# Kernel optimization log

Measured on AMD Instinct MI355X. Metric: run time of the kernel, lower is better.

## Reference

```python
import jax, jax.numpy as jnp
import numpy as np

N, E, IN, H = 10000, 50000, 32, 64


def setup_inputs() -> dict:
    key = jax.random.key(0)
    ks = jax.random.split(key, 12)
    s = lambda k, sh, sc=0.1: jax.random.normal(k, sh, dtype=jnp.float32) * sc
    return {
        "x": jax.random.normal(ks[0], (N, IN), dtype=jnp.float32),
        "edge_index": jax.random.randint(ks[1], (2, E), 0, N),
        "edge_attr": jax.random.uniform(ks[2], (E, 4), dtype=jnp.float32),
        "lin0_w": s(ks[3], (IN, H)),
        "lin0_b": jnp.zeros((H,), jnp.float32),
        "nn_w": s(ks[4], (4, H * H), 0.05),
        "nn_b": jnp.zeros((H * H,), jnp.float32),
        "root_w": s(ks[5], (H, H)),
        "conv_b": jnp.zeros((H,), jnp.float32),
        "gru_w_ih": s(ks[6], (3 * H, H)),
        "gru_w_hh": s(ks[7], (3 * H, H)),
        "gru_b_ih": jnp.zeros((3 * H,), jnp.float32),
        "gru_b_hh": jnp.zeros((3 * H,), jnp.float32),
    }


def reference(x, edge_index, edge_attr, lin0_w, lin0_b, nn_w, nn_b, root_w,
              conv_b, gru_w_ih, gru_w_hh, gru_b_ih, gru_b_hh):
    src, dst = edge_index[0], edge_index[1]
    # part == 'R': initial embedding
    out = jax.nn.relu(x @ lin0_w + lin0_b)  # [N, H]
    # Edge-conditioned weights are identical across the 3 iterations -> compute once.
    theta = (edge_attr @ nn_w + nn_b).reshape(E, H, H)  # per-edge [in, out]
    h = out  # GRU hidden init = out (h = out.unsqueeze(0))
    for _ in range(3):
        # NNConv: gather -> per-edge matmul -> scatter-add, plus root weight & bias
        msg = jnp.einsum('ei,eio->eo', out[src], theta)            # [E, H]
        agg = jax.ops.segment_sum(msg, dst, num_segments=N)        # [N, H]
        m = jax.nn.relu(agg + out @ root_w + conv_b)               # [N, H]
        # torch.nn.GRU single step (seq_len=1)
        gi = m @ gru_w_ih.T + gru_b_ih                             # [N, 3H]
        gh = h @ gru_w_hh.T + gru_b_hh                             # [N, 3H]
        i_r, i_z, i_n = jnp.split(gi, 3, axis=-1)
        h_r, h_z, h_n = jnp.split(gh, 3, axis=-1)
        r = jax.nn.sigmoid(i_r + h_r)
        z = jax.nn.sigmoid(i_z + h_z)
        n = jnp.tanh(i_n + r * h_n)
        h = (1.0 - z) * n + z * h
        out = h
    return out
```

## Files before the change

kernel.cpp:

```cpp
#include <hip/hip_runtime.h>


#define CAP 24
#define PACKB 96

using bf16x8 = __attribute__((ext_vector_type(8))) short;
using f32x4  = __attribute__((ext_vector_type(4))) float;

__device__ __forceinline__ float sigmoidf_(float x) { return 1.0f / (1.0f + __expf(-x)); }
__device__ __forceinline__ float tanhf_(float x) { return 2.0f / (1.0f + __expf(-2.0f * x)) - 1.0f; }
__device__ __forceinline__ unsigned short bf16r(float f) {
    unsigned u = __float_as_uint(f);
    return (unsigned short)((u + 0x7fffu + ((u >> 16) & 1u)) >> 16);
}
__device__ __forceinline__ unsigned bf16pk(float lo, float hi) {
    return (unsigned)bf16r(lo) | ((unsigned)bf16r(hi) << 16);
}

__global__ __launch_bounds__(256) void combo_k(const float* __restrict__ x,
                                               const float* __restrict__ w0,
                                               const float* __restrict__ b0,
                                               const float* __restrict__ nn_w,
                                               const float* __restrict__ nn_b,
                                               const float* __restrict__ root_w,
                                               const float* __restrict__ w_ih,
                                               const float* __restrict__ w_hh,
                                               unsigned* __restrict__ Wpk,
                                               float* __restrict__ h,
                                               int* __restrict__ dcnt, int N) {
    const int bid = blockIdx.x, tid = threadIdx.x;
    if (bid < PACKB) {
        int idx = bid * 256 + tid;
        int l = (idx >> 2) & 63, p = idx & 3;
        int kq = ((l >> 4) << 3) + 2 * p;
        float v0, v1;
        if (idx < 12288) {
            int f = idx >> 8;
            int ct = f / 12, s = f % 12;
            int k = 32 * s + kq;
            int col = 16 * ct + (l & 15);
            int c = k >> 6, j = k & 63;
            const float* base = (c < 4) ? nn_w + c * 4096 : (c == 4) ? nn_b : root_w;
            v0 = base[j * 64 + col];
            v1 = base[(j + 1) * 64 + col];
        } else {
            int idx2 = idx - 12288;
            int ts = idx2 >> 8;
            int g = ts >> 4, ct = (ts >> 2) & 3, s = ts & 3;
            int k = 32 * s + kq;
            int col = 16 * ct + (l & 15);
            const float* src = (k < 64) ? w_ih : w_hh;
            int kk = k & 63;
            v0 = src[(g * 64 + col) * 64 + kk];
            v1 = src[(g * 64 + col) * 64 + kk + 1];
        }
        Wpk[idx] = bf16pk(v0, v1);
    } else {
        int gid = (bid - PACKB) * 256 + tid;
        int gsz = (gridDim.x - PACKB) * 256;
        for (int i = gid; i < N; i += gsz) dcnt[i] = 0;
        for (int idx = gid; idx < N * 64; idx += gsz) {
            int n = idx >> 6, l = idx & 63;
            float acc = b0[l];
#pragma unroll
            for (int j = 0; j < 32; ++j) acc = fmaf(x[n * 32 + j], w0[j * 64 + l], acc);
            h[idx] = fmaxf(acc, 0.0f);
        }
    }
}

__global__ __launch_bounds__(256) void fillell_k(const int* __restrict__ ei,
                                                 const float4* __restrict__ ea,
                                                 int* __restrict__ dcnt,
                                                 int* __restrict__ esrc,
                                                 float4* __restrict__ eattr, int E) {
    int e = blockIdx.x * 256 + threadIdx.x;
    if (e >= E) return;
    int d = ei[E + e];
    int pos = atomicAdd(dcnt + d, 1);
    if (pos < CAP) {
        esrc[d * CAP + pos] = ei[e];
        eattr[d * CAP + pos] = ea[e];
    }
}

__global__ __launch_bounds__(256, 2) void iter_k(const float* __restrict__ h_old,
                                                 float* __restrict__ h_new,
                                                 const int* __restrict__ dcnt,
                                                 const int* __restrict__ esrc,
                                                 const float4* __restrict__ eattr,
                                                 const unsigned* __restrict__ Wpk,
                                                 const float* __restrict__ conv_b,
                                                 const float* __restrict__ b_ih,
                                                 const float* __restrict__ b_hh,
                                                 float* __restrict__ out_final, int N) {
    __shared__ unsigned short A1[16 * 384];
    __shared__ unsigned short AC[16 * 128];
    const int tid = threadIdx.x;
    const int n0 = blockIdx.x * 16;
    const int lane = tid & 63, wv = tid >> 6;

    bf16x8 wb[12], wc[12];
#pragma unroll
    for (int s = 0; s < 12; ++s)
        wb[s] = *(const bf16x8*)(Wpk + (wv * 12 + s) * 256 + lane * 4);
#pragma unroll
    for (int t = 0; t < 12; ++t) {
        int g = t >> 2, s = t & 3;
        wc[t] = *(const bf16x8*)(Wpk + 12288 + ((g * 4 + wv) * 4 + s) * 256 + lane * 4);
    }

    {
        int r = tid >> 4, q = tid & 15;
        int n = n0 + r;
        float4 hv = (n < N) ? *(const float4*)(h_old + (size_t)n * 64 + q * 4)
                            : make_float4(0.f, 0.f, 0.f, 0.f);
        uint2 pp = make_uint2(bf16pk(hv.x, hv.y), bf16pk(hv.z, hv.w));
        int sg1 = (40 + (q >> 1)) ^ (r & 7);
        *(uint2*)(A1 + r * 384 + sg1 * 8 + (q & 1) * 4) = pp;
        int sg2 = (8 + (q >> 1)) ^ (r & 7);
        *(uint2*)(AC + r * 128 + sg2 * 8 + (q & 1) * 4) = pp;
    }

#pragma unroll
    for (int i = 0; i < 4; ++i) {
        int r = wv * 4 + i;
        int n = n0 + r;
        float g0 = 0.f, g1 = 0.f, g2 = 0.f, g3 = 0.f, g4 = 0.f;
        if (n < N) {
            int deg = min(dcnt[n], CAP);
            int base = n * CAP;
            int t = 0;
            for (; t + 2 <= deg; t += 2) {
                int s0 = esrc[base + t], s1 = esrc[base + t + 1];
                float4 a0 = eattr[base + t], a1 = eattr[base + t + 1];
                float v0 = h_old[(size_t)s0 * 64 + lane];
                float v1 = h_old[(size_t)s1 * 64 + lane];
                g0 = fmaf(a0.x, v0, g0); g1 = fmaf(a0.y, v0, g1);
                g2 = fmaf(a0.z, v0, g2); g3 = fmaf(a0.w, v0, g3); g4 += v0;
                g0 = fmaf(a1.x, v1, g0); g1 = fmaf(a1.y, v1, g1);
                g2 = fmaf(a1.z, v1, g2); g3 = fmaf(a1.w, v1, g3); g4 += v1;
            }
            if (t < deg) {
                int s0 = esrc[base + t];
                float4 a0 = eattr[base + t];
                float v0 = h_old[(size_t)s0 * 64 + lane];
                g0 = fmaf(a0.x, v0, g0); g1 = fmaf(a0.y, v0, g1);
                g2 = fmaf(a0.z, v0, g2); g3 = fmaf(a0.w, v0, g3); g4 += v0;
            }
        }
        int x7 = r & 7, gl = lane >> 3, ge = lane & 7;
        A1[r * 384 + ((gl) ^ x7) * 8 + ge] = (unsigned short)bf16r(g0);
        A1[r * 384 + ((8 + gl) ^ x7) * 8 + ge] = (unsigned short)bf16r(g1);
        A1[r * 384 + ((16 + gl) ^ x7) * 8 + ge] = (unsigned short)bf16r(g2);
        A1[r * 384 + ((24 + gl) ^ x7) * 8 + ge] = (unsigned short)bf16r(g3);
        A1[r * 384 + ((32 + gl) ^ x7) * 8 + ge] = (unsigned short)bf16r(g4);
    }
    __syncthreads();

    const int arow = lane & 15;
    const int kblk = (lane >> 4) * 8;
    const int x7r = arow & 7;

    f32x4 accB = {0.f, 0.f, 0.f, 0.f};
#pragma unroll
    for (int s = 0; s < 12; ++s) {
        int k = 32 * s + kblk;
        bf16x8 af = *(const bf16x8*)(A1 + arow * 384 + ((k >> 3) ^ x7r) * 8);
        accB = __builtin_amdgcn_mfma_f32_16x16x32_bf16(af, wb[s], accB, 0, 0, 0);
    }

    const int mcol = wv * 16 + arow;
    const int rbase = (lane >> 4) * 4;
    {
        float cb = conv_b[mcol];
#pragma unroll
        for (int i = 0; i < 4; ++i) {
            int r = rbase + i;
            float mv = fmaxf(accB[i] + cb, 0.f);
            AC[r * 128 + ((mcol >> 3) ^ (r & 7)) * 8 + (mcol & 7)] =
                (unsigned short)bf16r(mv);
        }
    }
    __syncthreads();

    bf16x8 ac[4];
#pragma unroll
    for (int s = 0; s < 4; ++s) {
        int k = 32 * s + kblk;
        ac[s] = *(const bf16x8*)(AC + arow * 128 + ((k >> 3) ^ x7r) * 8);
    }
    f32x4 aR = {0.f, 0.f, 0.f, 0.f}, aZ = aR, aNi = aR, aNh = aR;
#pragma unroll
    for (int s = 0; s < 4; ++s)
        aR = __builtin_amdgcn_mfma_f32_16x16x32_bf16(ac[s], wc[s], aR, 0, 0, 0);
#pragma unroll
    for (int s = 0; s < 4; ++s)
        aZ = __builtin_amdgcn_mfma_f32_16x16x32_bf16(ac[s], wc[4 + s], aZ, 0, 0, 0);
    aNi = __builtin_amdgcn_mfma_f32_16x16x32_bf16(ac[0], wc[8], aNi, 0, 0, 0);
    aNi = __builtin_amdgcn_mfma_f32_16x16x32_bf16(ac[1], wc[9], aNi, 0, 0, 0);
    aNh = __builtin_amdgcn_mfma_f32_16x16x32_bf16(ac[2], wc[10], aNh, 0, 0, 0);
    aNh = __builtin_amdgcn_mfma_f32_16x16x32_bf16(ac[3], wc[11], aNh, 0, 0, 0);

    const int col = mcol;
    const float brz = b_ih[col] + b_hh[col];
    const float bzz = b_ih[64 + col] + b_hh[64 + col];
    const float bni = b_ih[128 + col];
    const float bnh = b_hh[128 + col];
#pragma unroll
    for (int i = 0; i < 4; ++i) {
        int n = n0 + rbase + i;
        if (n >= N) continue;
        float hv = h_old[(size_t)n * 64 + col];
        float rg = sigmoidf_(aR[i] + brz);
        float zg = sigmoidf_(aZ[i] + bzz);
        float ng = tanhf_(aNi[i] + bni + rg * (aNh[i] + bnh));
        float hn = (1.f - zg) * ng + zg * hv;
        h_new[(size_t)n * 64 + col] = hn;
        if (out_final) out_final[(size_t)n * 64 + col] = hn;
    }
}

extern "C" void kernel_launch(void* const* d_in, const int* in_sizes, int n_in,
                              void* d_out, int out_size, void* d_ws, size_t ws_size,
                              hipStream_t stream) {
    const float* x      = (const float*)d_in[0];
    const int*   ei     = (const int*)d_in[1];
    const float* ea     = (const float*)d_in[2];
    const float* lin0_w = (const float*)d_in[3];
    const float* lin0_b = (const float*)d_in[4];
    const float* nn_w   = (const float*)d_in[5];
    const float* nn_b   = (const float*)d_in[6];
    const float* root_w = (const float*)d_in[7];
    const float* conv_b = (const float*)d_in[8];
    const float* gw_ih  = (const float*)d_in[9];
    const float* gw_hh  = (const float*)d_in[10];
    const float* gb_ih  = (const float*)d_in[11];
    const float* gb_hh  = (const float*)d_in[12];

    const int N = in_sizes[0] / 32;
    const int E = in_sizes[1] / 2;

    float4*   eattr = (float4*)d_ws;
    float*    hA    = (float*)(eattr + (size_t)N * CAP);
    float*    hB    = hA + (size_t)N * 64;
    unsigned* Wpk   = (unsigned*)(hB + (size_t)N * 64);
    int*      esrc  = (int*)(Wpk + 24576);
    int*      dcnt  = esrc + (size_t)N * CAP;

    const int lin0_blocks = (N * 64 + 255) / 256;
    combo_k<<<PACKB + lin0_blocks, 256, 0, stream>>>(x, lin0_w, lin0_b, nn_w, nn_b,
                                                     root_w, gw_ih, gw_hh, Wpk, hA,
                                                     dcnt, N);
    fillell_k<<<(E + 255) / 256, 256, 0, stream>>>(ei, (const float4*)ea, dcnt,
                                                   esrc, eattr, E);

    const int TB = (N + 15) / 16;
    float* hbuf[2] = {hA, hB};
    for (int it = 0; it < 3; ++it) {
        iter_k<<<TB, 256, 0, stream>>>(hbuf[it & 1], hbuf[(it + 1) & 1], dcnt, esrc,
                                       eattr, Wpk, conv_b, gb_ih, gb_hh,
                                       (it == 2) ? (float*)d_out : nullptr, N);
    }
}
```

Before: 142.4 us.

## Interleave 4-node gathers, defer weight-fragment loads, vectorize lin0

The edge-gather loop now walks all four of a wave's destination nodes in lockstep, so each step keeps four independent global loads in flight instead of handling one node at a time. The MFMA weight fragments are loaded just before the matmul that uses them rather than at kernel entry, which lowers peak register pressure and lets launch bounds rise to three blocks per SIMD. The lin0 embedding in the setup kernel now produces four outputs per thread using float4 loads and stores. Lockstep gathering wastes lanes' work when node degrees differ, and the later weight loads are now exposed latency on the critical path.

```diff
diff --git a/kernel.cpp b/kernel.cpp
--- a/kernel.cpp
+++ b/kernel.cpp
@@ -59,12 +59,25 @@
         int gid = (bid - PACKB) * 256 + tid;
         int gsz = (gridDim.x - PACKB) * 256;
         for (int i = gid; i < N; i += gsz) dcnt[i] = 0;
-        for (int idx = gid; idx < N * 64; idx += gsz) {
-            int n = idx >> 6, l = idx & 63;
-            float acc = b0[l];
-#pragma unroll
-            for (int j = 0; j < 32; ++j) acc = fmaf(x[n * 32 + j], w0[j * 64 + l], acc);
-            h[idx] = fmaxf(acc, 0.0f);
+        for (int idx = gid; idx < N * 16; idx += gsz) {
+            int n = idx >> 4, q = idx & 15;
+            const float4* xr = (const float4*)(x + (size_t)n * 32);
+            float4 acc = *(const float4*)(b0 + q * 4);
+#pragma unroll
+            for (int j4 = 0; j4 < 8; ++j4) {
+                float4 xv = xr[j4];
+                const float4 w0r = *(const float4*)(w0 + (j4 * 4 + 0) * 64 + q * 4);
+                const float4 w1r = *(const float4*)(w0 + (j4 * 4 + 1) * 64 + q * 4);
+                const float4 w2r = *(const float4*)(w0 + (j4 * 4 + 2) * 64 + q * 4);
+                const float4 w3r = *(const float4*)(w0 + (j4 * 4 + 3) * 64 + q * 4);
+                acc.x = fmaf(xv.x, w0r.x, fmaf(xv.y, w1r.x, fmaf(xv.z, w2r.x, fmaf(xv.w, w3r.x, acc.x))));
+                acc.y = fmaf(xv.x, w0r.y, fmaf(xv.y, w1r.y, fmaf(xv.z, w2r.y, fmaf(xv.w, w3r.y, acc.y))));
+                acc.z = fmaf(xv.x, w0r.z, fmaf(xv.y, w1r.z, fmaf(xv.z, w2r.z, fmaf(xv.w, w3r.z, acc.z))));
+                acc.w = fmaf(xv.x, w0r.w, fmaf(xv.y, w1r.w, fmaf(xv.z, w2r.w, fmaf(xv.w, w3r.w, acc.w))));
+            }
+            acc.x = fmaxf(acc.x, 0.f); acc.y = fmaxf(acc.y, 0.f);
+            acc.z = fmaxf(acc.z, 0.f); acc.w = fmaxf(acc.w, 0.f);
+            *(float4*)(h + (size_t)n * 64 + q * 4) = acc;
         }
     }
 }
@@ -84,7 +97,7 @@
     }
 }
 
-__global__ __launch_bounds__(256, 2) void iter_k(const float* __restrict__ h_old,
+__global__ __launch_bounds__(256, 3) void iter_k(const float* __restrict__ h_old,
                                                  float* __restrict__ h_new,
                                                  const int* __restrict__ dcnt,
                                                  const int* __restrict__ esrc,
@@ -100,16 +113,6 @@
     const int n0 = blockIdx.x * 16;
     const int lane = tid & 63, wv = tid >> 6;
 
-    bf16x8 wb[12], wc[12];
-#pragma unroll
-    for (int s = 0; s < 12; ++s)
-        wb[s] = *(const bf16x8*)(Wpk + (wv * 12 + s) * 256 + lane * 4);
-#pragma unroll
-    for (int t = 0; t < 12; ++t) {
-        int g = t >> 2, s = t & 3;
-        wc[t] = *(const bf16x8*)(Wpk + 12288 + ((g * 4 + wv) * 4 + s) * 256 + lane * 4);
-    }
-
     {
         int r = tid >> 4, q = tid & 15;
         int n = n0 + r;
@@ -122,40 +125,57 @@
         *(uint2*)(AC + r * 128 + sg2 * 8 + (q & 1) * 4) = pp;
     }
 
-#pragma unroll
-    for (int i = 0; i < 4; ++i) {
-        int r = wv * 4 + i;
-        int n = n0 + r;
-        float g0 = 0.f, g1 = 0.f, g2 = 0.f, g3 = 0.f, g4 = 0.f;
-        if (n < N) {
-            int deg = min(dcnt[n], CAP);
-            int base = n * CAP;
-            int t = 0;
-            for (; t + 2 <= deg; t += 2) {
-                int s0 = esrc[base + t], s1 = esrc[base + t + 1];
-                float4 a0 = eattr[base + t], a1 = eattr[base + t + 1];
-                float v0 = h_old[(size_t)s0 * 64 + lane];
-                float v1 = h_old[(size_t)s1 * 64 + lane];
-                g0 = fmaf(a0.x, v0, g0); g1 = fmaf(a0.y, v0, g1);
-                g2 = fmaf(a0.z, v0, g2); g3 = fmaf(a0.w, v0, g3); g4 += v0;
-                g0 = fmaf(a1.x, v1, g0); g1 = fmaf(a1.y, v1, g1);
-                g2 = fmaf(a1.z, v1, g2); g3 = fmaf(a1.w, v1, g3); g4 += v1;
+    {
+        int deg[4], base[4];
+#pragma unroll
+        for (int i = 0; i < 4; ++i) {
+            int n = n0 + wv * 4 + i;
+            deg[i] = (n < N) ? min(dcnt[n], CAP) : 0;
+            base[i] = n * CAP;
+        }
+        float g[4][5];
+#pragma unroll
+        for (int i = 0; i < 4; ++i)
+#pragma unroll
+            for (int c = 0; c < 5; ++c) g[i][c] = 0.f;
+        int maxd = max(max(deg[0], deg[1]), max(deg[2], deg[3]));
+        for (int s = 0; s < maxd; ++s) {
+            float4 at[4];
+            float v[4];
+#pragma unroll
+            for (int i = 0; i < 4; ++i) {
+                bool ok = (s < deg[i]);
+                int src = ok ? esrc[base[i] + s] : 0;
+                at[i] = ok ? eattr[base[i] + s] : make_float4(0.f, 0.f, 0.f, 0.f);
+                v[i] = ok ? h_old[(size_t)src * 64 + lane] : 0.f;
             }
-            if (t < deg) {
-                int s0 = esrc[base + t];
-                float4 a0 = eattr[base + t];
-                float v0 = h_old[(size_t)s0 * 64 + lane];
-                g0 = fmaf(a0.x, v0, g0); g1 = fmaf(a0.y, v0, g1);
-                g2 = fmaf(a0.z, v0, g2); g3 = fmaf(a0.w, v0, g3); g4 += v0;
+#pragma unroll
+            for (int i = 0; i < 4; ++i) {
+                g[i][0] = fmaf(at[i].x, v[i], g[i][0]);
+                g[i][1] = fmaf(at[i].y, v[i], g[i][1]);
+                g[i][2] = fmaf(at[i].z, v[i], g[i][2]);
+                g[i][3] = fmaf(at[i].w, v[i], g[i][3]);
+                g[i][4] += v[i];
             }
         }
-        int x7 = r & 7, gl = lane >> 3, ge = lane & 7;
-        A1[r * 384 + ((gl) ^ x7) * 8 + ge] = (unsigned short)bf16r(g0);
-        A1[r * 384 + ((8 + gl) ^ x7) * 8 + ge] = (unsigned short)bf16r(g1);
-        A1[r * 384 + ((16 + gl) ^ x7) * 8 + ge] = (unsigned short)bf16r(g2);
-        A1[r * 384 + ((24 + gl) ^ x7) * 8 + ge] = (unsigned short)bf16r(g3);
-        A1[r * 384 + ((32 + gl) ^ x7) * 8 + ge] = (unsigned short)bf16r(g4);
-    }
+        int gl = lane >> 3, ge = lane & 7;
+#pragma unroll
+        for (int i = 0; i < 4; ++i) {
+            int r = wv * 4 + i;
+            int x7 = r & 7;
+            A1[r * 384 + (gl ^ x7) * 8 + ge] = (unsigned short)bf16r(g[i][0]);
+            A1[r * 384 + ((8 + gl) ^ x7) * 8 + ge] = (unsigned short)bf16r(g[i][1]);
+            A1[r * 384 + ((16 + gl) ^ x7) * 8 + ge] = (unsigned short)bf16r(g[i][2]);
+            A1[r * 384 + ((24 + gl) ^ x7) * 8 + ge] = (unsigned short)bf16r(g[i][3]);
+            A1[r * 384 + ((32 + gl) ^ x7) * 8 + ge] = (unsigned short)bf16r(g[i][4]);
+        }
+    }
+
+    bf16x8 wb[12];
+#pragma unroll
+    for (int s = 0; s < 12; ++s)
+        wb[s] = *(const bf16x8*)(Wpk + (wv * 12 + s) * 256 + lane * 4);
+
     __syncthreads();
 
     const int arow = lane & 15;
@@ -168,6 +188,13 @@
         int k = 32 * s + kblk;
         bf16x8 af = *(const bf16x8*)(A1 + arow * 384 + ((k >> 3) ^ x7r) * 8);
         accB = __builtin_amdgcn_mfma_f32_16x16x32_bf16(af, wb[s], accB, 0, 0, 0);
+    }
+
+    bf16x8 wc[12];
+#pragma unroll
+    for (int t = 0; t < 12; ++t) {
+        int g = t >> 2, s = t & 3;
+        wc[t] = *(const bf16x8*)(Wpk + 12288 + ((g * 4 + wv) * 4 + s) * 256 + lane * 4);
     }
 
     const int mcol = wv * 16 + arow;
@@ -248,7 +275,7 @@
     int*      esrc  = (int*)(Wpk + 24576);
     int*      dcnt  = esrc + (size_t)N * CAP;
 
-    const int lin0_blocks = (N * 64 + 255) / 256;
+    const int lin0_blocks = (N * 16 + 255) / 256;
     combo_k<<<PACKB + lin0_blocks, 256, 0, stream>>>(x, lin0_w, lin0_b, nn_w, nn_b,
                                                      root_w, gw_ih, gw_hh, Wpk, hA,
                                                      dcnt, N);
```

After: 144.4 us. No clear change (+1.4%).
